# Kernel optimization log

Measured on AMD Instinct MI355X. Metric: run time of the kernel, lower is better.

The kernel has to match this reference:

```python
import jax, jax.numpy as jnp
import numpy as np

N = 20000        # atoms
NEIGH = 12       # neighbors per atom
BSTEPS = 40      # bond GBF steps, range [0, 8]
ASTEPS = 20      # angle GBF steps, range [-1, 1]
H = 64           # hidden size
NCLS = 2         # n_classification
NCRYS = 20       # crystals (contiguous blocks of 1000 atoms)
NREL = 3         # edge relation types


def gbf(data, dmin, dmax, steps):
    # Gaussian basis expansion: exp(-(d - mu)^2 / gamma^2), gamma = (max-min)/steps
    filters = jnp.linspace(dmin, dmax, steps)
    gamma = (dmax - dmin) / steps
    return jnp.exp(-((data[..., None] - filters) ** 2) / gamma ** 2)


def rgcn(x, src, dst, etype, W_rel, W_root, b):
    # RGCNConv (PyG default): out = x @ W_root + b + sum_r mean_{j in N_r(i)} x_j @ W_r
    out = x @ W_root + b
    for r in range(NREL):
        w = (etype == r).astype(x.dtype)                     # [E]
        msg = (x @ W_rel[r])[src] * w[:, None]               # transform-then-gather: [E, H]
        s = jax.ops.segment_sum(msg, dst, num_segments=x.shape[0])
        c = jax.ops.segment_sum(w, dst, num_segments=x.shape[0])
        out = out + s / jnp.maximum(c, 1.0)[:, None]
    return out


def _forward(bond_fea, angle_fea, species, nbr_idx, crys_idx,
             W1b_rel, W1b_root, b1b, W1a_rel, W1a_root, b1a,
             W2b_rel, W2b_root, b2b, W2a_rel, W2a_root, b2a,
             fc_W, fc_b):
    n = bond_fea.shape[0]
    src = jnp.repeat(jnp.arange(n, dtype=jnp.int32), NEIGH)  # edge sources
    dst = nbr_idx.reshape(-1)                                # edge targets
    etype = species[src] + species[dst]                      # 0/1/2 per species pair

    edge_fea = gbf(bond_fea, 0.0, 8.0, BSTEPS).reshape(n, -1)      # [N, 480]
    ang_fea = gbf(angle_fea, -1.0, 1.0, ASTEPS).reshape(n, -1)     # [N, 2880]

    bf = jax.nn.relu(rgcn(edge_fea, src, dst, etype, W1b_rel, W1b_root, b1b))
    af = jax.nn.relu(rgcn(ang_fea, src, dst, etype, W1a_rel, W1a_root, b1a))
    # dropout treated as identity (eval/deterministic reference)
    bf = jax.nn.relu(rgcn(bf, src, dst, etype, W2b_rel, W2b_root, b2b))
    af = jax.nn.relu(rgcn(af, src, dst, etype, W2a_rel, W2a_root, b2a))

    feat = jnp.concatenate([bf, af], axis=1)                 # [N, 128]

    # pool: mean over contiguous [start, end) ranges per crystal
    starts = crys_idx[:, 0]
    crys_id = jnp.searchsorted(starts, jnp.arange(n), side='right') - 1
    sums = jax.ops.segment_sum(feat, crys_id, num_segments=NCRYS)
    counts = (crys_idx[:, 1] - crys_idx[:, 0]).astype(feat.dtype)[:, None]
    pooled = sums / counts                                   # [NCRYS, 128]

    return pooled @ fc_W + fc_b                              # [NCRYS, NCLS]


def setup_inputs() -> dict:
    key = jax.random.key(0)
    ks = jax.random.split(key, 20)
    bond_fea = jax.random.uniform(ks[0], (N, NEIGH), dtype=jnp.float32) * 8.0
    angle_fea = jax.random.uniform(ks[1], (N, NEIGH, NEIGH), dtype=jnp.float32) * 2.0 - 1.0
    species = jax.random.randint(ks[2], (N,), 0, 2, dtype=jnp.int32)
    nbr_idx = jax.random.randint(ks[3], (N, NEIGH), 0, N, dtype=jnp.int32)
    starts = jnp.arange(NCRYS, dtype=jnp.int32) * (N // NCRYS)
    crys_idx = jnp.stack([starts, starts + (N // NCRYS)], axis=1)

    def w(k, shape, fan_in):
        return jax.random.normal(k, shape, dtype=jnp.float32) / np.sqrt(fan_in)

    in_b = BSTEPS * NEIGH            # 480
    in_a = ASTEPS * NEIGH * NEIGH    # 2880
    return {
        'bond_fea': bond_fea, 'angle_fea': angle_fea, 'species': species,
        'nbr_idx': nbr_idx, 'crys_idx': crys_idx,
        'W1b_rel': w(ks[4], (NREL, in_b, H), in_b), 'W1b_root': w(ks[5], (in_b, H), in_b),
        'b1b': jnp.zeros((H,), jnp.float32),
        'W1a_rel': w(ks[6], (NREL, in_a, H), in_a), 'W1a_root': w(ks[7], (in_a, H), in_a),
        'b1a': jnp.zeros((H,), jnp.float32),
        'W2b_rel': w(ks[8], (NREL, H, H), H), 'W2b_root': w(ks[9], (H, H), H),
        'b2b': jnp.zeros((H,), jnp.float32),
        'W2a_rel': w(ks[10], (NREL, H, H), H), 'W2a_root': w(ks[11], (H, H), H),
        'b2a': jnp.zeros((H,), jnp.float32),
        'fc_W': w(ks[12], (2 * H, NCLS), 2 * H), 'fc_b': jnp.zeros((NCLS,), jnp.float32),
    }


def reference(bond_fea, angle_fea, species, nbr_idx, crys_idx,
              W1b_rel, W1b_root, b1b, W1a_rel, W1a_root, b1a,
              W2b_rel, W2b_root, b2b, W2a_rel, W2a_root, b2a,
              fc_W, fc_b):
    return _forward(bond_fea, angle_fea, species, nbr_idx, crys_idx,
                    W1b_rel, W1b_root, b1b, W1a_rel, W1a_root, b1a,
                    W2b_rel, W2b_root, b2b, W2a_rel, W2a_root, b2a,
                    fc_W, fc_b)
```

## Files before the change

### kernel.cpp

```cpp
#include <hip/hip_runtime.h>

#define NN 20000
#define NNP 20096
#define NEIGH 12
#define NCRYS 20
#define MT2 1256
#define NSUB 16

typedef __bf16 bf16x8 __attribute__((ext_vector_type(8)));
typedef __bf16 bf16x4 __attribute__((ext_vector_type(4)));
typedef float f32x4 __attribute__((ext_vector_type(4)));

__device__ __forceinline__ float readlane_f(float v, int l) {
    return __int_as_float(__builtin_amdgcn_readlane(__float_as_int(v), l));
}

__device__ __forceinline__ void pack_one(const float* Wrel, const float* Wroot,
                                         __bf16* Wp, int K, int idx) {
    int k = idx >> 8, n = idx & 255;
    int r = n >> 6, h = n & 63;
    float v = (r < 3) ? Wrel[((size_t)r * K + k) * 64 + h] : Wroot[(size_t)k * 64 + h];
    int kt = k >> 5, k8 = (k >> 3) & 3, j = k & 7, nt = n >> 4, ni = n & 15;
    Wp[((((size_t)kt * 16 + nt) * 4 + k8) * 16 + ni) * 8 + j] = (__bf16)v;
}

__device__ __forceinline__ void pack_cat(const float* Wrel, const float* Wroot,
                                         __bf16* Wp, int idx) {
    int k4 = idx >> 6, n = idx & 63;
    int q = k4 >> 6, kk = k4 & 63;
    float v = q ? Wrel[(((q - 1) * 64 + kk) * 64) + n] : Wroot[kk * 64 + n];
    int kt = k4 >> 5, k8 = (k4 >> 3) & 3, j = k4 & 7, nt = n >> 4, ni = n & 15;
    Wp[((((size_t)kt * 4 + nt) * 4 + k8) * 16 + ni) * 8 + j] = (__bf16)v;
}

__global__ __launch_bounds__(256) void setup_kernel(
    const int* __restrict__ species, const int* __restrict__ nbr,
    int* __restrict__ adj, int* __restrict__ deg,
    const float* __restrict__ W1b_rel, const float* __restrict__ W1b_root,
    const float* __restrict__ W1a_rel, const float* __restrict__ W1a_root,
    const float* __restrict__ W2b_rel, const float* __restrict__ W2b_root,
    const float* __restrict__ W2a_rel, const float* __restrict__ W2a_root,
    __bf16* __restrict__ Wp1b, __bf16* __restrict__ Wp1a,
    __bf16* __restrict__ Wp2b, __bf16* __restrict__ Wp2a,
    const float* __restrict__ bond, const float* __restrict__ angle,
    float* __restrict__ bondT, float* __restrict__ angleT) {
    __shared__ float ls[64 * 145];
    const int bx = blockIdx.x, tid = threadIdx.x;
    if (bx < 938) {
        int e = bx * 256 + tid;
        if (e < NN * NEIGH) {
            int i = e / NEIGH;
            int d = nbr[e];
            int r = species[i] + species[d];
            int slot = atomicAdd(&deg[d], 1);
            if (slot < 64) adj[(size_t)d * 64 + slot] = i | (r << 28);
        }
    } else if (bx < 938 + 256) {
        const int S0 = 480 * 256;
        const int S1 = S0 + 2880 * 256;
        const int S2 = S1 + 16384;
        const int S3 = S2 + 16384;
        const int S4 = S3 + 8192;
        const int S5 = S4 + 49152;
        for (int idx = (bx - 938) * 256 + tid; idx < S5; idx += 256 * 256) {
            if (idx < S0)       pack_one(W1b_rel, W1b_root, Wp1b, 480, idx);
            else if (idx < S1)  pack_one(W1a_rel, W1a_root, Wp1a, 2880, idx - S0);
            else if (idx < S2)  pack_cat(W2b_rel, W2b_root, Wp2b, idx - S1);
            else if (idx < S3)  pack_cat(W2a_rel, W2a_root, Wp2a, idx - S2);
            else if (idx < S4)  Wp1b[480 * 256 + (idx - S3)] = (__bf16)0.f;
            else                Wp1a[2880 * 256 + (idx - S4)] = (__bf16)0.f;
        }
    } else {
        int tb = bx - 1194;
        if (tb < 314) {
            int m0 = tb * 64;
            for (int idx = tid; idx < 64 * 144; idx += 256) {
                int mm = idx / 144, j = idx - mm * 144;
                int m = m0 + mm;
                ls[mm * 145 + j] = (m < NN) ? angle[(size_t)m * 144 + j] : 0.f;
            }
            __syncthreads();
            for (int idx = tid; idx < 156 * 64; idx += 256) {
                int j = idx >> 6, mm = idx & 63;
                angleT[(size_t)j * NNP + m0 + mm] = (j < 144) ? ls[mm * 145 + j] : 0.f;
            }
        } else {
            int m0 = (tb - 314) * 64;
            for (int idx = tid; idx < 64 * 12; idx += 256) {
                int mm = idx / 12, j = idx - mm * 12;
                int m = m0 + mm;
                ls[mm * 13 + j] = (m < NN) ? bond[(size_t)m * 12 + j] : 0.f;
            }
            __syncthreads();
            for (int idx = tid; idx < 16 * 64; idx += 256) {
                int j = idx >> 6, mm = idx & 63;
                bondT[(size_t)j * NNP + m0 + mm] = (j < 12) ? ls[mm * 13 + j] : 0.f;
            }
        }
    }
}

template <int MODE, typename OUT_T>
__device__ __forceinline__ void gemm1_body(const float* __restrict__ xT,
                                           const __bf16* __restrict__ Wp,
                                           OUT_T* __restrict__ Y, int mb,
                                           __bf16* __restrict__ Al,
                                           int ph0, int nph) {
    constexpr int DIVN = (MODE == 0) ? 40 : 20;
    constexpr int ADDJ = 64 / DIVN;
    constexpr int ADDS = 64 % DIVN;
    constexpr float F0 = (MODE == 0) ? 0.f : -1.f;
    constexpr float FS = (MODE == 0) ? (8.f / 39.f) : (2.f / 19.f);
    constexpr float NG2 = ((MODE == 0) ? -25.f : -100.f) * 1.44269504f;
    const float C  = __builtin_amdgcn_exp2f(2.f * NG2 * FS * FS);
    const float P1 = NG2 * FS * FS;
    const float P2 = -2.f * NG2 * FS;

    const int tid = threadIdx.x;
    const int lane = tid & 63, wv = tid >> 6;
    const int m0 = mb * 64;
    const int smt = tid >> 7;
    const int sk8 = (tid >> 5) & 3;
    const int smi = (tid >> 1) & 15;
    const int sjh = (tid & 1) * 4;
    const int sgm = m0 + smt * 16 + smi;
    const int kk0 = sk8 * 8 + sjh;
    const int swoff = (((smt * 4 + sk8) * 16 + smi) * 8 + sjh);
    const int k8b = lane >> 4, nib = lane & 15;

    f32x4 acc[4][2] = {};

    const int k00 = ph0 * 64 + kk0;
    const int k01 = ph0 * 64 + 32 + kk0;
    const float* pA0 = xT + (size_t)(k00 / DIVN) * NNP + sgm;
    const float* pA1 = xT + (size_t)(k01 / DIVN) * NNP + sgm;
    int sL0 = k00 % DIVN, sL1 = k01 % DIVN;
    int sS0 = sL0, sS1 = sL1;

    const bf16x8* pB0 = (const bf16x8*)Wp + (size_t)ph0 * 2048 +
                        ((size_t)(2 * wv) * 4 + k8b) * 16 + nib;
    const bf16x8* pB1 = pB0 + 1024;

    bf16x8 bEv[4], bOd[4];

    auto advL = [&]() {
        sL0 += ADDS;
        if (sL0 >= DIVN) { sL0 -= DIVN; pA0 += (size_t)(ADDJ + 1) * NNP; } else pA0 += (size_t)ADDJ * NNP;
        sL1 += ADDS;
        if (sL1 >= DIVN) { sL1 -= DIVN; pA1 += (size_t)(ADDJ + 1) * NNP; } else pA1 += (size_t)ADDJ * NNP;
    };
    auto advS = [&]() {
        sS0 += ADDS; if (sS0 >= DIVN) sS0 -= DIVN;
        sS1 += ADDS; if (sS1 >= DIVN) sS1 -= DIVN;
    };
    auto loadB = [&](bf16x8* d) {
        d[0] = pB0[0]; d[1] = pB0[64]; d[2] = pB1[0]; d[3] = pB1[64];
        pB0 += 2048; pB1 += 2048;
    };
    auto stage = [&](float a0, float a1, __bf16* dst) {
        float d0 = a0 - (F0 + (float)sS0 * FS);
        float d1 = a1 - (F0 + (float)sS1 * FS);
        float e0a = __builtin_amdgcn_exp2f(NG2 * d0 * d0);
        float q0a = __builtin_amdgcn_exp2f(fmaf(P2, d0, P1));
        float e0b = __builtin_amdgcn_exp2f(NG2 * d1 * d1);
        float q0b = __builtin_amdgcn_exp2f(fmaf(P2, d1, P1));
        float e1a = e0a * q0a, q1a = q0a * C;
        float e2a = e1a * q1a, e3a = e2a * q1a * C;
        float e1b = e0b * q0b, q1b = q0b * C;
        float e2b = e1b * q1b, e3b = e2b * q1b * C;
        bf16x4 v0, v1;
        v0[0] = (__bf16)e0a; v0[1] = (__bf16)e1a; v0[2] = (__bf16)e2a; v0[3] = (__bf16)e3a;
        v1[0] = (__bf16)e0b; v1[1] = (__bf16)e1b; v1[2] = (__bf16)e2b; v1[3] = (__bf16)e3b;
        *(bf16x4*)&dst[swoff] = v0;
        *(bf16x4*)&dst[2048 + swoff] = v1;
    };
    auto mma = [&](const __bf16* Ab, const bf16x8* bc) {
        bf16x8 af[4], ag[4];
#pragma unroll
        for (int t4 = 0; t4 < 4; ++t4) {
            af[t4] = *(const bf16x8*)&Ab[(((((t4 << 2) + k8b) << 4) + nib) << 3)];
            ag[t4] = *(const bf16x8*)&Ab[2048 + (((((t4 << 2) + k8b) << 4) + nib) << 3)];
        }
#pragma unroll
        for (int i = 0; i < 4; ++i) {
            acc[i][0] = __builtin_amdgcn_mfma_f32_16x16x32_bf16(af[i], bc[0], acc[i][0], 0, 0, 0);
            acc[i][1] = __builtin_amdgcn_mfma_f32_16x16x32_bf16(af[i], bc[1], acc[i][1], 0, 0, 0);
        }
#pragma unroll
        for (int i = 0; i < 4; ++i) {
            acc[i][0] = __builtin_amdgcn_mfma_f32_16x16x32_bf16(ag[i], bc[2], acc[i][0], 0, 0, 0);
            acc[i][1] = __builtin_amdgcn_mfma_f32_16x16x32_bf16(ag[i], bc[3], acc[i][1], 0, 0, 0);
        }
    };

    float a00 = pA0[0], a01 = pA1[0]; advL();
    float aN0 = pA0[0], aN1 = pA1[0]; advL();
    stage(a00, a01, Al); advS();
    loadB(bEv);
    loadB(bOd);
    __syncthreads();

    const int np2 = nph >> 1;
    for (int p2 = 0; p2 < np2; ++p2) {
        const bool last = (p2 == np2 - 1);
        mma(Al, bEv);
        if (!last) loadB(bEv);
        stage(aN0, aN1, Al + 4096); advS();
        if (!last) { aN0 = pA0[0]; aN1 = pA1[0]; advL(); }
        __syncthreads();
        mma(Al + 4096, bOd);
        if (!last) {
            loadB(bOd);
            stage(aN0, aN1, Al); advS();
            aN0 = pA0[0]; aN1 = pA1[0]; advL();
        }
        __syncthreads();
    }

    const int mrow0 = m0 + ((lane >> 4) << 2);
    const int ncol = (wv << 5) + nib;
#pragma unroll
    for (int i = 0; i < 4; ++i)
#pragma unroll
        for (int j = 0; j < 2; ++j)
#pragma unroll
            for (int v = 0; v < 4; ++v) {
                int m = mrow0 + i * 16 + v;
                if (m < NN) Y[(size_t)m * 256 + ncol + j * 16] = (OUT_T)acc[i][j][v];
            }
}

__global__ __launch_bounds__(512, 4) void mega_gemm1(const float* __restrict__ bondT,
                                                     const float* __restrict__ angleT,
                                                     const __bf16* __restrict__ Wp1b,
                                                     const __bf16* __restrict__ Wp1a,
                                                     __bf16* __restrict__ Yb,
                                                     float* __restrict__ Ya1,
                                                     float* __restrict__ Ya2) {
    __shared__ __align__(16) __bf16 Al[2 * 4096];
    int bx = blockIdx.x;
    if (bx < 314)       gemm1_body<1, float>(angleT, Wp1a, Ya1, bx, Al, 0, 24);
    else if (bx < 628)  gemm1_body<1, float>(angleT, Wp1a, Ya2, bx - 314, Al, 24, 24);
    else                gemm1_body<0, __bf16>(bondT, Wp1b, Yb, bx - 628, Al, 0, 8);
}

__global__ __launch_bounds__(256) void addY(const float* __restrict__ Y1,
                                            const float* __restrict__ Y2,
                                            __bf16* __restrict__ Yo) {
    size_t i = ((size_t)blockIdx.x * 256 + threadIdx.x) * 8;
    f32x4 a0 = *(const f32x4*)&Y1[i], a1 = *(const f32x4*)&Y1[i + 4];
    f32x4 b0 = *(const f32x4*)&Y2[i], b1 = *(const f32x4*)&Y2[i + 4];
    bf16x8 o;
#pragma unroll
    for (int c = 0; c < 4; ++c) {
        o[c] = (__bf16)(a0[c] + b0[c]);
        o[4 + c] = (__bf16)(a1[c] + b1[c]);
    }
    *(bf16x8*)&Yo[i] = o;
}

__global__ __launch_bounds__(256) void agg1(const __bf16* __restrict__ Yb,
                                            const __bf16* __restrict__ Ya,
                                            const int* __restrict__ adj,
                                            const int* __restrict__ deg,
                                            const float* __restrict__ biasb,
                                            const float* __restrict__ biasa,
                                            __bf16* __restrict__ Hb,
                                            __bf16* __restrict__ Ha) {
    int node = blockIdx.x * 4 + (threadIdx.x >> 6);
    int h = threadIdx.x & 63;
    if (node >= NN) return;
    int dg = min(deg[node], 64);
    int e = adj[(size_t)node * 64 + h];
    bool val = h < dg;
    int r = e >> 28;
    unsigned long long bl0 = __ballot(val && r == 0);
    unsigned long long bl1 = __ballot(val && r == 1);
    unsigned long long bl2 = __ballot(val && r == 2);
    int c0 = __popcll(bl0), c1 = __popcll(bl1), c2 = __popcll(bl2);
    float w = val ? 1.f / (float)((r == 0) ? c0 : (r == 1) ? c1 : c2) : 0.f;
    float sb = 0.f, sa = 0.f;
    if (dg > 0) {
        int e0 = __builtin_amdgcn_readfirstlane(e);
        int ec = val ? e : e0;
        for (int k0 = 0; k0 < dg; k0 += 16) {
            float vb[16], va[16];
#pragma unroll
            for (int i = 0; i < 16; ++i) {
                int ek = __builtin_amdgcn_readlane(ec, k0 + i);
                size_t base = (size_t)(ek & 0x0FFFFFFF) * 256 + (ek >> 28) * 64 + h;
                vb[i] = (float)Yb[base];
                va[i] = (float)Ya[base];
            }
#pragma unroll
            for (int i = 0; i < 16; ++i) {
                float wk = readlane_f(w, k0 + i);
                sb = fmaf(vb[i], wk, sb);
                sa = fmaf(va[i], wk, sa);
            }
        }
    }
    float ob = (float)Yb[(size_t)node * 256 + 192 + h] + biasb[h] + sb;
    float oa = (float)Ya[(size_t)node * 256 + 192 + h] + biasa[h] + sa;
    Hb[(size_t)node * 64 + h] = (__bf16)fmaxf(ob, 0.f);
    Ha[(size_t)node * 64 + h] = (__bf16)fmaxf(oa, 0.f);
}

__global__ __launch_bounds__(256) void agg2(const __bf16* __restrict__ Hb,
                                            const __bf16* __restrict__ Ha,
                                            const int* __restrict__ adj,
                                            const int* __restrict__ deg,
                                            __bf16* __restrict__ Apb,
                                            __bf16* __restrict__ Apa) {
    int node = blockIdx.x * 4 + (threadIdx.x >> 6);
    int h = threadIdx.x & 63;
    float hb = 0.f, rb0 = 0.f, rb1 = 0.f, rb2 = 0.f;
    float ha = 0.f, ra0 = 0.f, ra1 = 0.f, ra2 = 0.f;
    if (node < NN) {
        int dg = min(deg[node], 64);
        int e = adj[(size_t)node * 64 + h];
        bool val = h < dg;
        int r = e >> 28;
        unsigned long long bl0 = __ballot(val && r == 0);
        unsigned long long bl1 = __ballot(val && r == 1);
        unsigned long long bl2 = __ballot(val && r == 2);
        int c0 = __popcll(bl0), c1 = __popcll(bl1), c2 = __popcll(bl2);
        float sb0 = 0.f, sb1 = 0.f, sb2 = 0.f;
        float sa0 = 0.f, sa1 = 0.f, sa2 = 0.f;
        hb = (float)Hb[(size_t)node * 64 + h];
        ha = (float)Ha[(size_t)node * 64 + h];
        if (dg > 0) {
            int e0 = __builtin_amdgcn_readfirstlane(e);
            int ec = val ? e : e0;
            for (int k0 = 0; k0 < dg; k0 += 16) {
                float vb[16], va[16];
#pragma unroll
                for (int i = 0; i < 16; ++i) {
                    int ek = __builtin_amdgcn_readlane(ec, k0 + i);
                    size_t base = (size_t)(ek & 0x0FFFFFFF) * 64 + h;
                    vb[i] = (float)Hb[base];
                    va[i] = (float)Ha[base];
                }
#pragma unroll
                for (int i = 0; i < 16; ++i) {
                    int kk = k0 + i;
                    if (kk < dg) {
                        int rr = __builtin_amdgcn_readlane(ec, kk) >> 28;
                        if (rr == 0)      { sb0 += vb[i]; sa0 += va[i]; }
                        else if (rr == 1) { sb1 += vb[i]; sa1 += va[i]; }
                        else              { sb2 += vb[i]; sa2 += va[i]; }
                    }
                }
            }
        }
        float i0 = 1.f / fmaxf((float)c0, 1.f);
        float i1 = 1.f / fmaxf((float)c1, 1.f);
        float i2 = 1.f / fmaxf((float)c2, 1.f);
        rb0 = sb0 * i0; rb1 = sb1 * i1; rb2 = sb2 * i2;
        ra0 = sa0 * i0; ra1 = sa1 * i1; ra2 = sa2 * i2;
    }
    int mt = node >> 4, mi = node & 15;
    float vb4[4] = {hb, rb0, rb1, rb2};
    float va4[4] = {ha, ra0, ra1, ra2};
#pragma unroll
    for (int q = 0; q < 4; ++q) {
        int K4 = q * 64 + h;
        int kt = K4 >> 5, k8 = (K4 >> 3) & 3, j = K4 & 7;
        size_t off = ((((size_t)kt * MT2 + mt) * 4 + k8) * 16 + mi) * 8 + j;
        Apb[off] = (__bf16)vb4[q];
        Apa[off] = (__bf16)va4[q];
    }
}

__global__ __launch_bounds__(256) void gemm3(const __bf16* __restrict__ Apb,
                                             const __bf16* __restrict__ Apa,
                                             const __bf16* __restrict__ Wpb,
                                             const __bf16* __restrict__ Wpa,
                                             const float* __restrict__ bb,
                                             const float* __restrict__ ba,
                                             const int* __restrict__ crys,
                                             float* __restrict__ pooled) {
    const int ch = blockIdx.y;
    const bf16x8* Ag = (const bf16x8*)(ch ? Apa : Apb);
    const bf16x8* Bg = (const bf16x8*)(ch ? Wpa : Wpb);
    const float* bias = ch ? ba : bb;
    const int base = ch ? 64 : 0;
    const int tid = threadIdx.x, lane = tid & 63, wv = tid >> 6;
    const int mt0 = blockIdx.x * 8 + wv * 2;
    const int k8b = lane >> 4, nib = lane & 15;
    f32x4 acc[2][4] = {};
#pragma unroll
    for (int kt = 0; kt < 8; ++kt) {
        bf16x8 a0 = Ag[(((size_t)kt * MT2 + mt0) * 4 + k8b) * 16 + nib];
        bf16x8 a1 = Ag[(((size_t)kt * MT2 + mt0 + 1) * 4 + k8b) * 16 + nib];
        bf16x8 b0 = Bg[(((size_t)kt * 4 + 0) * 4 + k8b) * 16 + nib];
        bf16x8 b1 = Bg[(((size_t)kt * 4 + 1) * 4 + k8b) * 16 + nib];
        bf16x8 b2 = Bg[(((size_t)kt * 4 + 2) * 4 + k8b) * 16 + nib];
        bf16x8 b3 = Bg[(((size_t)kt * 4 + 3) * 4 + k8b) * 16 + nib];
        acc[0][0] = __builtin_amdgcn_mfma_f32_16x16x32_bf16(a0, b0, acc[0][0], 0, 0, 0);
        acc[0][1] = __builtin_amdgcn_mfma_f32_16x16x32_bf16(a0, b1, acc[0][1], 0, 0, 0);
        acc[0][2] = __builtin_amdgcn_mfma_f32_16x16x32_bf16(a0, b2, acc[0][2], 0, 0, 0);
        acc[0][3] = __builtin_amdgcn_mfma_f32_16x16x32_bf16(a0, b3, acc[0][3], 0, 0, 0);
        acc[1][0] = __builtin_amdgcn_mfma_f32_16x16x32_bf16(a1, b0, acc[1][0], 0, 0, 0);
        acc[1][1] = __builtin_amdgcn_mfma_f32_16x16x32_bf16(a1, b1, acc[1][1], 0, 0, 0);
        acc[1][2] = __builtin_amdgcn_mfma_f32_16x16x32_bf16(a1, b2, acc[1][2], 0, 0, 0);
        acc[1][3] = __builtin_amdgcn_mfma_f32_16x16x32_bf16(a1, b3, acc[1][3], 0, 0, 0);
    }
    const int rowoff = ((lane >> 4) << 2);
#pragma unroll
    for (int i = 0; i < 2; ++i)
#pragma unroll
        for (int v = 0; v < 4; ++v) {
            int m = (mt0 + i) * 16 + rowoff + v;
            if (m < NN) {
                int cc = 0;
#pragma unroll
                for (int t = 1; t < NCRYS; ++t) cc += (m >= crys[t * 2]) ? 1 : 0;
                int sub = ((m >> 4) + ((m >> 2) & 3)) & (NSUB - 1);
                float* pb = &pooled[((size_t)cc * NSUB + sub) * 128 + base];
#pragma unroll
                for (int j = 0; j < 4; ++j) {
                    int n = j * 16 + nib;
                    float o = fmaxf(acc[i][j][v] + bias[n], 0.f);
                    atomicAdd(&pb[n], o);
                }
            }
        }
}

__global__ void final2(const float* __restrict__ pooled, const int* __restrict__ crys,
                       const float* __restrict__ fcW, const float* __restrict__ fcb,
                       float* __restrict__ out) {
    int c = blockIdx.x >> 1, o = blockIdx.x & 1;
    int l = threadIdx.x;
    float cnt = (float)(crys[c * 2 + 1] - crys[c * 2]);
    float sb = 0.f, sa = 0.f;
    for (int s = 0; s < NSUB; ++s) {
        sb += pooled[((size_t)c * NSUB + s) * 128 + l];
        sa += pooled[((size_t)c * NSUB + s) * 128 + 64 + l];
    }
    float a = sb * fcW[l * 2 + o] + sa * fcW[(64 + l) * 2 + o];
    for (int s = 32; s > 0; s >>= 1) a += __shfl_down(a, s);
    if (l == 0) out[c * 2 + o] = a / cnt + fcb[o];
}

extern "C" void kernel_launch(void* const* d_in, const int* in_sizes, int n_in,
                              void* d_out, int out_size, void* d_ws, size_t ws_size,
                              hipStream_t stream) {
    const float* bond    = (const float*)d_in[0];
    const float* angle   = (const float*)d_in[1];
    const int*   species = (const int*)d_in[2];
    const int*   nbr     = (const int*)d_in[3];
    const int*   crys    = (const int*)d_in[4];
    const float* W1b_rel = (const float*)d_in[5];
    const float* W1b_root= (const float*)d_in[6];
    const float* b1b     = (const float*)d_in[7];
    const float* W1a_rel = (const float*)d_in[8];
    const float* W1a_root= (const float*)d_in[9];
    const float* b1a     = (const float*)d_in[10];
    const float* W2b_rel = (const float*)d_in[11];
    const float* W2b_root= (const float*)d_in[12];
    const float* b2b     = (const float*)d_in[13];
    const float* W2a_rel = (const float*)d_in[14];
    const float* W2a_root= (const float*)d_in[15];
    const float* b2a     = (const float*)d_in[16];
    const float* fcW     = (const float*)d_in[17];
    const float* fcb     = (const float*)d_in[18];
    float* out = (float*)d_out;

    char* ws = (char*)d_ws;
    size_t off = 0;
    auto alloc = [&](size_t bytes) {
        char* p = ws + off;
        off = (off + bytes + 255) & ~(size_t)255;
        return p;
    };
    __bf16* Wp1b = (__bf16*)alloc((size_t)512 * 256 * 2);
    __bf16* Wp1a = (__bf16*)alloc((size_t)3072 * 256 * 2);
    __bf16* Wp2b = (__bf16*)alloc((size_t)256 * 64 * 2);
    __bf16* Wp2a = (__bf16*)alloc((size_t)256 * 64 * 2);
    float*  bondT = (float*)alloc((size_t)16 * NNP * 4);
    float*  angleT= (float*)alloc((size_t)156 * NNP * 4);
    __bf16* Yb   = (__bf16*)alloc((size_t)NN * 256 * 2);
    __bf16* Ya   = (__bf16*)alloc((size_t)NN * 256 * 2);
    float*  Ya1  = (float*)alloc((size_t)NN * 256 * 4);
    float*  Ya2  = (float*)alloc((size_t)NN * 256 * 4);
    __bf16* Hrowb= (__bf16*)alloc((size_t)NNP * 64 * 2);
    __bf16* Hrowa= (__bf16*)alloc((size_t)NNP * 64 * 2);
    __bf16* Apb  = (__bf16*)alloc((size_t)8 * MT2 * 512 * 2);
    __bf16* Apa  = (__bf16*)alloc((size_t)8 * MT2 * 512 * 2);
    int*    adj  = (int*)alloc((size_t)NN * 64 * 4);
    int*    deg  = (int*)alloc((size_t)NN * 4);
    float*  pooled = (float*)alloc((size_t)NCRYS * NSUB * 128 * 4);

    hipMemsetAsync(deg, 0, (size_t)NN * 4, stream);
    hipMemsetAsync(pooled, 0, (size_t)NCRYS * NSUB * 128 * 4, stream);

    setup_kernel<<<1822, 256, 0, stream>>>(species, nbr, adj, deg,
                                           W1b_rel, W1b_root, W1a_rel, W1a_root,
                                           W2b_rel, W2b_root, W2a_rel, W2a_root,
                                           Wp1b, Wp1a, Wp2b, Wp2a,
                                           bond, angle, bondT, angleT);

    mega_gemm1<<<942, 512, 0, stream>>>(bondT, angleT, Wp1b, Wp1a, Yb, Ya1, Ya2);
    addY<<<2500, 256, 0, stream>>>(Ya1, Ya2, Ya);
    agg1<<<5024, 256, 0, stream>>>(Yb, Ya, adj, deg, b1b, b1a, Hrowb, Hrowa);
    agg2<<<5024, 256, 0, stream>>>(Hrowb, Hrowa, adj, deg, Apb, Apa);
    gemm3<<<dim3(157, 2), 256, 0, stream>>>(Apb, Apa, Wp2b, Wp2a, b2b, b2a, crys, pooled);
    final2<<<NCRYS * 2, 64, 0, stream>>>(pooled, crys, fcW, fcb, out);
}
```

Baseline: 233.2 us.

## Split adjacency lists per relation type to drop ballots and branchy accumulation

The graph setup now builds a separate adjacency list and degree counter for each (destination, relation) pair instead of one list whose entries carry the relation in their high bits. Both aggregation kernels then loop over the three lists in blocks of 8 neighbors, so the per-node ballot/popcount counting and the per-edge relation branch disappear. In exchange the adjacency buffer is three times larger, the atomic counters are spread over more slots, and each relation's final partial block is still loaded in full but only its valid entries are summed.

```diff
diff --git a/kernel.cpp b/kernel.cpp
--- a/kernel.cpp
+++ b/kernel.cpp
@@ -10,10 +10,6 @@
 typedef __bf16 bf16x8 __attribute__((ext_vector_type(8)));
 typedef __bf16 bf16x4 __attribute__((ext_vector_type(4)));
 typedef float f32x4 __attribute__((ext_vector_type(4)));
-
-__device__ __forceinline__ float readlane_f(float v, int l) {
-    return __int_as_float(__builtin_amdgcn_readlane(__float_as_int(v), l));
-}
 
 __device__ __forceinline__ void pack_one(const float* Wrel, const float* Wroot,
                                          __bf16* Wp, int K, int idx) {
@@ -35,7 +31,7 @@
 
 __global__ __launch_bounds__(256) void setup_kernel(
     const int* __restrict__ species, const int* __restrict__ nbr,
-    int* __restrict__ adj, int* __restrict__ deg,
+    int* __restrict__ adj3, int* __restrict__ deg3,
     const float* __restrict__ W1b_rel, const float* __restrict__ W1b_root,
     const float* __restrict__ W1a_rel, const float* __restrict__ W1a_root,
     const float* __restrict__ W2b_rel, const float* __restrict__ W2b_root,
@@ -52,8 +48,8 @@
             int i = e / NEIGH;
             int d = nbr[e];
             int r = species[i] + species[d];
-            int slot = atomicAdd(&deg[d], 1);
-            if (slot < 64) adj[(size_t)d * 64 + slot] = i | (r << 28);
+            int slot = atomicAdd(&deg3[d * 3 + r], 1);
+            if (slot < 64) adj3[(((size_t)d * 3 + r) << 6) + slot] = i;
         }
     } else if (bx < 938 + 256) {
         const int S0 = 480 * 256;
@@ -261,8 +257,8 @@
 
 __global__ __launch_bounds__(256) void agg1(const __bf16* __restrict__ Yb,
                                             const __bf16* __restrict__ Ya,
-                                            const int* __restrict__ adj,
-                                            const int* __restrict__ deg,
+                                            const int* __restrict__ adj3,
+                                            const int* __restrict__ deg3,
                                             const float* __restrict__ biasb,
                                             const float* __restrict__ biasa,
                                             __bf16* __restrict__ Hb,
@@ -270,98 +266,107 @@
     int node = blockIdx.x * 4 + (threadIdx.x >> 6);
     int h = threadIdx.x & 63;
     if (node >= NN) return;
-    int dg = min(deg[node], 64);
-    int e = adj[(size_t)node * 64 + h];
-    bool val = h < dg;
-    int r = e >> 28;
-    unsigned long long bl0 = __ballot(val && r == 0);
-    unsigned long long bl1 = __ballot(val && r == 1);
-    unsigned long long bl2 = __ballot(val && r == 2);
-    int c0 = __popcll(bl0), c1 = __popcll(bl1), c2 = __popcll(bl2);
-    float w = val ? 1.f / (float)((r == 0) ? c0 : (r == 1) ? c1 : c2) : 0.f;
-    float sb = 0.f, sa = 0.f;
-    if (dg > 0) {
-        int e0 = __builtin_amdgcn_readfirstlane(e);
-        int ec = val ? e : e0;
-        for (int k0 = 0; k0 < dg; k0 += 16) {
-            float vb[16], va[16];
-#pragma unroll
-            for (int i = 0; i < 16; ++i) {
-                int ek = __builtin_amdgcn_readlane(ec, k0 + i);
-                size_t base = (size_t)(ek & 0x0FFFFFFF) * 256 + (ek >> 28) * 64 + h;
-                vb[i] = (float)Yb[base];
-                va[i] = (float)Ya[base];
-            }
-#pragma unroll
-            for (int i = 0; i < 16; ++i) {
-                float wk = readlane_f(w, k0 + i);
-                sb = fmaf(vb[i], wk, sb);
-                sa = fmaf(va[i], wk, sa);
-            }
-        }
-    }
-    float ob = (float)Yb[(size_t)node * 256 + 192 + h] + biasb[h] + sb;
-    float oa = (float)Ya[(size_t)node * 256 + 192 + h] + biasa[h] + sa;
+    int c[3], ec[3];
+#pragma unroll
+    for (int r = 0; r < 3; ++r) {
+        int er = adj3[(((size_t)node * 3 + r) << 6) + h];
+        c[r] = min(deg3[node * 3 + r], 64);
+        int e0 = __builtin_amdgcn_readfirstlane(er);
+        ec[r] = (h < c[r]) ? er : e0;
+    }
+    float sb[3] = {0.f, 0.f, 0.f}, sa[3] = {0.f, 0.f, 0.f};
+    for (int b = 0; b < 64; b += 8) {
+        if (b >= c[0] && b >= c[1] && b >= c[2]) break;
+        float vb[3][8], va[3][8];
+#pragma unroll
+        for (int r = 0; r < 3; ++r)
+            if (b < c[r]) {
+#pragma unroll
+                for (int i = 0; i < 8; ++i) {
+                    int ek = __builtin_amdgcn_readlane(ec[r], b + i);
+                    size_t base = (size_t)ek * 256 + (r << 6) + h;
+                    vb[r][i] = (float)Yb[base];
+                    va[r][i] = (float)Ya[base];
+                }
+            }
+#pragma unroll
+        for (int r = 0; r < 3; ++r)
+            if (b < c[r]) {
+#pragma unroll
+                for (int i = 0; i < 8; ++i)
+                    if (b + i < c[r]) {
+                        sb[r] += vb[r][i];
+                        sa[r] += va[r][i];
+                    }
+            }
+    }
+    float ob = (float)Yb[(size_t)node * 256 + 192 + h] + biasb[h];
+    float oa = (float)Ya[(size_t)node * 256 + 192 + h] + biasa[h];
+#pragma unroll
+    for (int r = 0; r < 3; ++r) {
+        float inv = 1.f / fmaxf((float)c[r], 1.f);
+        ob = fmaf(sb[r], inv, ob);
+        oa = fmaf(sa[r], inv, oa);
+    }
     Hb[(size_t)node * 64 + h] = (__bf16)fmaxf(ob, 0.f);
     Ha[(size_t)node * 64 + h] = (__bf16)fmaxf(oa, 0.f);
 }
 
 __global__ __launch_bounds__(256) void agg2(const __bf16* __restrict__ Hb,
                                             const __bf16* __restrict__ Ha,
-                                            const int* __restrict__ adj,
-                                            const int* __restrict__ deg,
+                                            const int* __restrict__ adj3,
+                                            const int* __restrict__ deg3,
                                             __bf16* __restrict__ Apb,
                                             __bf16* __restrict__ Apa) {
     int node = blockIdx.x * 4 + (threadIdx.x >> 6);
     int h = threadIdx.x & 63;
-    float hb = 0.f, rb0 = 0.f, rb1 = 0.f, rb2 = 0.f;
-    float ha = 0.f, ra0 = 0.f, ra1 = 0.f, ra2 = 0.f;
+    float vb4[4] = {0.f, 0.f, 0.f, 0.f};
+    float va4[4] = {0.f, 0.f, 0.f, 0.f};
     if (node < NN) {
-        int dg = min(deg[node], 64);
-        int e = adj[(size_t)node * 64 + h];
-        bool val = h < dg;
-        int r = e >> 28;
-        unsigned long long bl0 = __ballot(val && r == 0);
-        unsigned long long bl1 = __ballot(val && r == 1);
-        unsigned long long bl2 = __ballot(val && r == 2);
-        int c0 = __popcll(bl0), c1 = __popcll(bl1), c2 = __popcll(bl2);
-        float sb0 = 0.f, sb1 = 0.f, sb2 = 0.f;
-        float sa0 = 0.f, sa1 = 0.f, sa2 = 0.f;
-        hb = (float)Hb[(size_t)node * 64 + h];
-        ha = (float)Ha[(size_t)node * 64 + h];
-        if (dg > 0) {
-            int e0 = __builtin_amdgcn_readfirstlane(e);
-            int ec = val ? e : e0;
-            for (int k0 = 0; k0 < dg; k0 += 16) {
-                float vb[16], va[16];
-#pragma unroll
-                for (int i = 0; i < 16; ++i) {
-                    int ek = __builtin_amdgcn_readlane(ec, k0 + i);
-                    size_t base = (size_t)(ek & 0x0FFFFFFF) * 64 + h;
-                    vb[i] = (float)Hb[base];
-                    va[i] = (float)Ha[base];
-                }
-#pragma unroll
-                for (int i = 0; i < 16; ++i) {
-                    int kk = k0 + i;
-                    if (kk < dg) {
-                        int rr = __builtin_amdgcn_readlane(ec, kk) >> 28;
-                        if (rr == 0)      { sb0 += vb[i]; sa0 += va[i]; }
-                        else if (rr == 1) { sb1 += vb[i]; sa1 += va[i]; }
-                        else              { sb2 += vb[i]; sa2 += va[i]; }
+        int c[3], ec[3];
+#pragma unroll
+        for (int r = 0; r < 3; ++r) {
+            int er = adj3[(((size_t)node * 3 + r) << 6) + h];
+            c[r] = min(deg3[node * 3 + r], 64);
+            int e0 = __builtin_amdgcn_readfirstlane(er);
+            ec[r] = (h < c[r]) ? er : e0;
+        }
+        float sb[3] = {0.f, 0.f, 0.f}, sa[3] = {0.f, 0.f, 0.f};
+        for (int b = 0; b < 64; b += 8) {
+            if (b >= c[0] && b >= c[1] && b >= c[2]) break;
+            float vb[3][8], va[3][8];
+#pragma unroll
+            for (int r = 0; r < 3; ++r)
+                if (b < c[r]) {
+#pragma unroll
+                    for (int i = 0; i < 8; ++i) {
+                        int ek = __builtin_amdgcn_readlane(ec[r], b + i);
+                        size_t base = (size_t)ek * 64 + h;
+                        vb[r][i] = (float)Hb[base];
+                        va[r][i] = (float)Ha[base];
                     }
                 }
-            }
-        }
-        float i0 = 1.f / fmaxf((float)c0, 1.f);
-        float i1 = 1.f / fmaxf((float)c1, 1.f);
-        float i2 = 1.f / fmaxf((float)c2, 1.f);
-        rb0 = sb0 * i0; rb1 = sb1 * i1; rb2 = sb2 * i2;
-        ra0 = sa0 * i0; ra1 = sa1 * i1; ra2 = sa2 * i2;
+#pragma unroll
+            for (int r = 0; r < 3; ++r)
+                if (b < c[r]) {
+#pragma unroll
+                    for (int i = 0; i < 8; ++i)
+                        if (b + i < c[r]) {
+                            sb[r] += vb[r][i];
+                            sa[r] += va[r][i];
+                        }
+                }
+        }
+        vb4[0] = (float)Hb[(size_t)node * 64 + h];
+        va4[0] = (float)Ha[(size_t)node * 64 + h];
+#pragma unroll
+        for (int r = 0; r < 3; ++r) {
+            float inv = 1.f / fmaxf((float)c[r], 1.f);
+            vb4[1 + r] = sb[r] * inv;
+            va4[1 + r] = sa[r] * inv;
+        }
     }
     int mt = node >> 4, mi = node & 15;
-    float vb4[4] = {hb, rb0, rb1, rb2};
-    float va4[4] = {ha, ra0, ra1, ra2};
 #pragma unroll
     for (int q = 0; q < 4; ++q) {
         int K4 = q * 64 + h;
@@ -489,14 +494,14 @@
     __bf16* Hrowa= (__bf16*)alloc((size_t)NNP * 64 * 2);
     __bf16* Apb  = (__bf16*)alloc((size_t)8 * MT2 * 512 * 2);
     __bf16* Apa  = (__bf16*)alloc((size_t)8 * MT2 * 512 * 2);
-    int*    adj  = (int*)alloc((size_t)NN * 64 * 4);
-    int*    deg  = (int*)alloc((size_t)NN * 4);
+    int*    adj3 = (int*)alloc((size_t)NN * 3 * 64 * 4);
+    int*    deg3 = (int*)alloc((size_t)NN * 3 * 4);
     float*  pooled = (float*)alloc((size_t)NCRYS * NSUB * 128 * 4);
 
-    hipMemsetAsync(deg, 0, (size_t)NN * 4, stream);
+    hipMemsetAsync(deg3, 0, (size_t)NN * 3 * 4, stream);
     hipMemsetAsync(pooled, 0, (size_t)NCRYS * NSUB * 128 * 4, stream);
 
-    setup_kernel<<<1822, 256, 0, stream>>>(species, nbr, adj, deg,
+    setup_kernel<<<1822, 256, 0, stream>>>(species, nbr, adj3, deg3,
                                            W1b_rel, W1b_root, W1a_rel, W1a_root,
                                            W2b_rel, W2b_root, W2a_rel, W2a_root,
                                            Wp1b, Wp1a, Wp2b, Wp2a,
@@ -504,8 +509,8 @@
 
     mega_gemm1<<<942, 512, 0, stream>>>(bondT, angleT, Wp1b, Wp1a, Yb, Ya1, Ya2);
     addY<<<2500, 256, 0, stream>>>(Ya1, Ya2, Ya);
-    agg1<<<5024, 256, 0, stream>>>(Yb, Ya, adj, deg, b1b, b1a, Hrowb, Hrowa);
-    agg2<<<5024, 256, 0, stream>>>(Hrowb, Hrowa, adj, deg, Apb, Apa);
+    agg1<<<5000, 256, 0, stream>>>(Yb, Ya, adj3, deg3, b1b, b1a, Hrowb, Hrowa);
+    agg2<<<5024, 256, 0, stream>>>(Hrowb, Hrowa, adj3, deg3, Apb, Apa);
     gemm3<<<dim3(157, 2), 256, 0, stream>>>(Apb, Apa, Wp2b, Wp2a, b2b, b2a, crys, pooled);
     final2<<<NCRYS * 2, 64, 0, stream>>>(pooled, crys, fcW, fcb, out);
 }
```

After: 243.7 us. 4.5% more time.
